# Kernel tuning notes

Measured on AMD Instinct MI355X. Metric: run time of the kernel, lower is better.

Reference implementation:

```python
import jax, jax.numpy as jnp
import numpy as np

N, IN_DIM, ERR_DIM, CAND, NR = 100000, 168, 24, 256, 4

def setup_inputs() -> dict:
    key = jax.random.key(0)
    k1, k2, k3, k4, k5 = jax.random.split(key, 5)
    return {
        "input": jax.random.normal(k1, (N, IN_DIM), dtype=jnp.float32),
        "error": jax.random.normal(k2, (N, ERR_DIM), dtype=jnp.float32),
        "weight_candidates": jax.random.normal(k3, (IN_DIM, CAND), dtype=jnp.float32),
        "bias_candidates": jax.random.normal(k4, (1, CAND), dtype=jnp.float32),
        "r": jax.random.uniform(k5, (NR,), dtype=jnp.float32),
    }

def reference(input, error, weight_candidates, bias_candidates, r):
    # candidates_state: [N, C] = sigmoid(X W + b)
    cand_state = jax.nn.sigmoid(input @ weight_candidates + bias_candidates)
    # E^T C: [D, C]; replaces per-(candidate,dim) tiny mm loop
    ec = jnp.einsum('nd,nc->dc', error, cand_state)
    # c^T c per candidate: [C]
    cc = jnp.sum(cand_state * cand_state, axis=0)
    # left_vector summed over dims: [C]
    left = jnp.sum(ec * ec, axis=0) / cc
    # sum over dims of e_dim^T e_dim: scalar
    ee = jnp.sum(error * error)
    # scores[idx, i] = sum_dim left - (1 - r_i) * right
    scores = left[:, None] - (1.0 - r)[None, :] * ee  # [C, NR]
    return scores
```

## Files before the change

kernel.cpp:

```cpp
#include <hip/hip_runtime.h>


#define N_ROWS 100000
#define IN_DIM 168
#define ERR_DIM 24
#define CAND 256

#define M_TILE 64
#define NT 1563
#define RBLKS 256
#define XT_STRIDE 200
#define ST_STRIDE 72
#define NCOPY 8

typedef __bf16 bf16;
typedef bf16 bf16x4 __attribute__((ext_vector_type(4)));
typedef bf16 bf16x8 __attribute__((ext_vector_type(8)));
typedef float f32x4 __attribute__((ext_vector_type(4)));

#define EC_F 0
#define CC_F 49152
#define EE_F 51200
#define ZERO_N 51456
#define WP_F 51712

__device__ __forceinline__ f32x4 mfma16(bf16x8 a, bf16x8 b, f32x4 c) {
    return __builtin_amdgcn_mfma_f32_16x16x32_bf16(a, b, c, 0, 0, 0);
}

__device__ __forceinline__ float fast_sigmoid(float x) {
    return __builtin_amdgcn_rcpf(1.0f + __expf(-x));
}

__global__ __launch_bounds__(256) void prep_kernel(const float* __restrict__ W,
                                                   bf16* __restrict__ wp,
                                                   float* __restrict__ zero_region) {
    int tid = blockIdx.x * 256 + threadIdx.x;
    for (int i = tid; i < ZERO_N; i += 6144) zero_region[i] = 0.0f;
    int ct  = tid / 384;
    int rem = tid % 384;
    int kt  = rem / 64;
    int l   = rem % 64;
    int c   = ct * 16 + (l & 15);
    int k0  = kt * 32 + (l >> 4) * 8;
    bf16x8 v;
#pragma unroll
    for (int j = 0; j < 8; ++j) {
        int k = k0 + j;
        float f = (k < IN_DIM) ? W[(size_t)k * CAND + c] : 0.0f;
        v[j] = (bf16)f;
    }
    *reinterpret_cast<bf16x8*>(wp + (size_t)tid * 8) = v;
}

__global__ __launch_bounds__(256) void fused_main(const float* __restrict__ X,
                                                  const float* __restrict__ E,
                                                  const float* __restrict__ B,
                                                  const bf16* __restrict__ wp,
                                                  float* __restrict__ ec_ws,
                                                  float* __restrict__ cc_ws,
                                                  float* __restrict__ ee_ws) {
    __shared__ bf16 XT[M_TILE * XT_STRIDE];
    __shared__ bf16 SigT[64 * ST_STRIDE];
    __shared__ bf16 ET[32 * ST_STRIDE];
    __shared__ float red[8];

    const int pid  = blockIdx.x;
    const int cg   = (pid >> 3) >> 5;
    const int rblk = (((pid >> 3) & 31) << 3) | (pid & 7);

    const int tid  = threadIdx.x;
    const int wave = tid >> 6;
    const int lane = tid & 63;
    const int lo   = lane & 15;
    const int hi   = lane >> 4;
    const int ct   = cg * 4 + wave;
    const int cand = ct * 16 + lo;

    bf16x8 wf[6];
#pragma unroll
    for (int kt = 0; kt < 6; ++kt)
        wf[kt] = *reinterpret_cast<const bf16x8*>(wp + (((size_t)(ct * 6 + kt)) * 64 + lane) * 8);
    const float bv = B[cand];

    f32x4 ec_acc[2];
    ec_acc[0] = (f32x4){0.f, 0.f, 0.f, 0.f};
    ec_acc[1] = (f32x4){0.f, 0.f, 0.f, 0.f};
    float cc_acc = 0.f;
    float ee_acc = 0.f;

    for (int i = tid; i < 8 * ST_STRIDE; i += 256)
        ET[(24 + i / ST_STRIDE) * ST_STRIDE + (i % ST_STRIDE)] = (bf16)0.0f;
    {
        bf16x4 z = {(bf16)0.f, (bf16)0.f, (bf16)0.f, (bf16)0.f};
        for (int i = tid; i < 64 * 6; i += 256) {
            int r = i / 6, p = i % 6;
            *reinterpret_cast<bf16x4*>(&XT[r * XT_STRIDE + IN_DIM + p * 4]) = z;
        }
    }

    f32x4 xr[11], er[2];

    auto issue_tile = [&](int tn) {
        const int row0n = tn * M_TILE;
        const bool tval = (tn < NT);
#pragma unroll
        for (int j = 0; j < 11; ++j) {
            int idx = tid + j * 256;
            int r = idx / 42, c4 = idx - r * 42;
            int gr = row0n + r;
            f32x4 v = {0.f, 0.f, 0.f, 0.f};
            if (tval && idx < 2688 && gr < N_ROWS)
                v = *reinterpret_cast<const f32x4*>(X + (size_t)gr * IN_DIM + c4 * 4);
            xr[j] = v;
        }
#pragma unroll
        for (int j = 0; j < 2; ++j) {
            int idx = tid + j * 256;
            int r = idx / 6, p = idx - r * 6;
            int gr = row0n + r;
            f32x4 v = {0.f, 0.f, 0.f, 0.f};
            if (tval && idx < 384 && gr < N_ROWS)
                v = *reinterpret_cast<const f32x4*>(E + (size_t)gr * ERR_DIM + p * 4);
            er[j] = v;
        }
    };

    issue_tile(rblk);

    for (int t = rblk; t < NT; t += RBLKS) {
        const int row0 = t * M_TILE;
        __syncthreads();

#pragma unroll
        for (int j = 0; j < 11; ++j) {
            int idx = tid + j * 256;
            if (idx < 2688) {
                int r = idx / 42, c4 = idx - r * 42;
                f32x4 v = xr[j];
                bf16x4 pk = {(bf16)v.x, (bf16)v.y, (bf16)v.z, (bf16)v.w};
                *reinterpret_cast<bf16x4*>(&XT[r * XT_STRIDE + c4 * 4]) = pk;
            }
        }
#pragma unroll
        for (int j = 0; j < 2; ++j) {
            int idx = tid + j * 256;
            if (idx < 384) {
                int r = idx / 6, p = idx - r * 6;
                f32x4 v = er[j];
                if (cg == 0)
                    ee_acc += v.x * v.x + v.y * v.y + v.z * v.z + v.w * v.w;
                int d0 = p * 4;
                ET[(d0 + 0) * ST_STRIDE + r] = (bf16)v.x;
                ET[(d0 + 1) * ST_STRIDE + r] = (bf16)v.y;
                ET[(d0 + 2) * ST_STRIDE + r] = (bf16)v.z;
                ET[(d0 + 3) * ST_STRIDE + r] = (bf16)v.w;
            }
        }
        __syncthreads();

        issue_tile(t + RBLKS);

        f32x4 acc[4];
#pragma unroll
        for (int mf = 0; mf < 4; ++mf) acc[mf] = (f32x4){0.f, 0.f, 0.f, 0.f};
#pragma unroll
        for (int kt = 0; kt < 6; ++kt) {
            bf16x8 a[4];
#pragma unroll
            for (int mf = 0; mf < 4; ++mf)
                a[mf] = *reinterpret_cast<const bf16x8*>(&XT[(mf * 16 + lo) * XT_STRIDE + kt * 32 + hi * 8]);
#pragma unroll
            for (int mf = 0; mf < 4; ++mf)
                acc[mf] = mfma16(a[mf], wf[kt], acc[mf]);
        }

#pragma unroll
        for (int mf = 0; mf < 4; ++mf) {
            const int rb = row0 + mf * 16 + hi * 4;
            f32x4 v = acc[mf];
            float s0 = fast_sigmoid(v.x + bv);
            float s1 = fast_sigmoid(v.y + bv);
            float s2 = fast_sigmoid(v.z + bv);
            float s3 = fast_sigmoid(v.w + bv);
            if (rb + 0 >= N_ROWS) s0 = 0.0f;
            if (rb + 1 >= N_ROWS) s1 = 0.0f;
            if (rb + 2 >= N_ROWS) s2 = 0.0f;
            if (rb + 3 >= N_ROWS) s3 = 0.0f;
            cc_acc += s0 * s0 + s1 * s1 + s2 * s2 + s3 * s3;
            bf16x4 pk = {(bf16)s0, (bf16)s1, (bf16)s2, (bf16)s3};
            *reinterpret_cast<bf16x4*>(&SigT[(wave * 16 + lo) * ST_STRIDE + mf * 16 + hi * 4]) = pk;
        }

#pragma unroll
        for (int kt2 = 0; kt2 < 2; ++kt2) {
            bf16x8 ea0 = *reinterpret_cast<const bf16x8*>(&ET[(0 * 16 + lo) * ST_STRIDE + kt2 * 32 + hi * 8]);
            bf16x8 ea1 = *reinterpret_cast<const bf16x8*>(&ET[(1 * 16 + lo) * ST_STRIDE + kt2 * 32 + hi * 8]);
            bf16x8 sb  = *reinterpret_cast<const bf16x8*>(&SigT[(wave * 16 + lo) * ST_STRIDE + kt2 * 32 + hi * 8]);
            ec_acc[0] = mfma16(ea0, sb, ec_acc[0]);
            ec_acc[1] = mfma16(ea1, sb, ec_acc[1]);
        }
    }

    const int copy = rblk & (NCOPY - 1);
#pragma unroll
    for (int rf = 0; rf < 2; ++rf)
#pragma unroll
        for (int rr = 0; rr < 4; ++rr) {
            int d = rf * 16 + hi * 4 + rr;
            if (d < ERR_DIM)
                atomicAdd(&ec_ws[copy * (ERR_DIM * CAND) + d * CAND + cand], ec_acc[rf][rr]);
        }
    {
        float v = cc_acc;
        v += __shfl_down(v, 32);
        v += __shfl_down(v, 16);
        if (lane < 16) atomicAdd(&cc_ws[copy * CAND + ct * 16 + lane], v);
    }
    if (cg == 0) {
#pragma unroll
        for (int off = 32; off > 0; off >>= 1) ee_acc += __shfl_down(ee_acc, off);
        if (lane == 0) red[wave] = ee_acc;
    }
    __syncthreads();
    if (cg == 0 && tid == 0) ee_ws[rblk] = red[0] + red[1] + red[2] + red[3];
}

__global__ __launch_bounds__(256) void finalize(const float* __restrict__ ec_ws,
                                                const float* __restrict__ cc_ws,
                                                const float* __restrict__ ee_ws,
                                                const float* __restrict__ r,
                                                float* __restrict__ out) {
    __shared__ float tmp[4];
    __shared__ float s_ee;
    int c = threadIdx.x;
    float p = ee_ws[c];
#pragma unroll
    for (int off = 32; off > 0; off >>= 1) p += __shfl_down(p, off);
    if ((c & 63) == 0) tmp[c >> 6] = p;
    __syncthreads();
    if (c == 0) s_ee = tmp[0] + tmp[1] + tmp[2] + tmp[3];
    __syncthreads();
    float ee = s_ee;
    float ccv = 0.f;
#pragma unroll
    for (int cp = 0; cp < NCOPY; ++cp) ccv += cc_ws[cp * CAND + c];
    float left = 0.f;
#pragma unroll
    for (int d = 0; d < ERR_DIM; ++d) {
        float v = 0.f;
#pragma unroll
        for (int cp = 0; cp < NCOPY; ++cp) v += ec_ws[cp * (ERR_DIM * CAND) + d * CAND + c];
        left += v * v;
    }
    left /= ccv;
#pragma unroll
    for (int i = 0; i < 4; ++i) out[c * 4 + i] = left - (1.0f - r[i]) * ee;
}

extern "C" void kernel_launch(void* const* d_in, const int* in_sizes, int n_in,
                              void* d_out, int out_size, void* d_ws, size_t ws_size,
                              hipStream_t stream) {
    const float* X = (const float*)d_in[0];
    const float* E = (const float*)d_in[1];
    const float* W = (const float*)d_in[2];
    const float* B = (const float*)d_in[3];
    const float* r = (const float*)d_in[4];

    float* wsf   = (float*)d_ws;
    float* ec_ws = wsf + EC_F;
    float* cc_ws = wsf + CC_F;
    float* ee_ws = wsf + EE_F;
    bf16*  wp    = (bf16*)(wsf + WP_F);

    prep_kernel<<<24, 256, 0, stream>>>(W, wp, wsf);
    fused_main<<<4 * RBLKS, 256, 0, stream>>>(X, E, B, wp, ec_ws, cc_ws, ee_ws);
    finalize<<<1, 256, 0, stream>>>(ec_ws, cc_ws, ee_ws, r, (float*)d_out);
}
```

Before: 136.3 us.

## Swap MFMA work split so each wave owns a row block across all candidates

Each wave now computes a 16-row slice for all 64 candidates of its group instead of 64 rows for 16 candidates. It keeps four candidate weight fragment sets in registers and reads one X fragment per k-step, which cuts LDS reads of the X tile by a factor of four. Because the sigmoid tile is now written across waves, a new barrier is added before the E^T·S MFMAs. Register pressure rises (24 bf16x8 weight fragments), which could lower occupancy.

```diff
diff --git a/kernel.cpp b/kernel.cpp
--- a/kernel.cpp
+++ b/kernel.cpp
@@ -74,19 +74,23 @@
     const int lane = tid & 63;
     const int lo   = lane & 15;
     const int hi   = lane >> 4;
-    const int ct   = cg * 4 + wave;
-    const int cand = ct * 16 + lo;
-
-    bf16x8 wf[6];
-#pragma unroll
-    for (int kt = 0; kt < 6; ++kt)
-        wf[kt] = *reinterpret_cast<const bf16x8*>(wp + (((size_t)(ct * 6 + kt)) * 64 + lane) * 8);
-    const float bv = B[cand];
+
+    bf16x8 wf[4][6];
+#pragma unroll
+    for (int cf = 0; cf < 4; ++cf)
+#pragma unroll
+        for (int kt = 0; kt < 6; ++kt)
+            wf[cf][kt] = *reinterpret_cast<const bf16x8*>(
+                wp + (((size_t)((cg * 4 + cf) * 6 + kt)) * 64 + lane) * 8);
+
+    float bv[4];
+#pragma unroll
+    for (int cf = 0; cf < 4; ++cf) bv[cf] = B[cg * 64 + cf * 16 + lo];
 
     f32x4 ec_acc[2];
     ec_acc[0] = (f32x4){0.f, 0.f, 0.f, 0.f};
     ec_acc[1] = (f32x4){0.f, 0.f, 0.f, 0.f};
-    float cc_acc = 0.f;
+    float cc_acc[4] = {0.f, 0.f, 0.f, 0.f};
     float ee_acc = 0.f;
 
     for (int i = tid; i < 8 * ST_STRIDE; i += 256)
@@ -100,7 +104,6 @@
     }
 
     f32x4 xr[11], er[2];
-
     auto issue_tile = [&](int tn) {
         const int row0n = tn * M_TILE;
         const bool tval = (tn < NT);
@@ -163,34 +166,36 @@
 
         f32x4 acc[4];
 #pragma unroll
-        for (int mf = 0; mf < 4; ++mf) acc[mf] = (f32x4){0.f, 0.f, 0.f, 0.f};
+        for (int cf = 0; cf < 4; ++cf) acc[cf] = (f32x4){0.f, 0.f, 0.f, 0.f};
 #pragma unroll
         for (int kt = 0; kt < 6; ++kt) {
-            bf16x8 a[4];
-#pragma unroll
-            for (int mf = 0; mf < 4; ++mf)
-                a[mf] = *reinterpret_cast<const bf16x8*>(&XT[(mf * 16 + lo) * XT_STRIDE + kt * 32 + hi * 8]);
-#pragma unroll
-            for (int mf = 0; mf < 4; ++mf)
-                acc[mf] = mfma16(a[mf], wf[kt], acc[mf]);
-        }
-
-#pragma unroll
-        for (int mf = 0; mf < 4; ++mf) {
-            const int rb = row0 + mf * 16 + hi * 4;
-            f32x4 v = acc[mf];
-            float s0 = fast_sigmoid(v.x + bv);
-            float s1 = fast_sigmoid(v.y + bv);
-            float s2 = fast_sigmoid(v.z + bv);
-            float s3 = fast_sigmoid(v.w + bv);
-            if (rb + 0 >= N_ROWS) s0 = 0.0f;
-            if (rb + 1 >= N_ROWS) s1 = 0.0f;
-            if (rb + 2 >= N_ROWS) s2 = 0.0f;
-            if (rb + 3 >= N_ROWS) s3 = 0.0f;
-            cc_acc += s0 * s0 + s1 * s1 + s2 * s2 + s3 * s3;
-            bf16x4 pk = {(bf16)s0, (bf16)s1, (bf16)s2, (bf16)s3};
-            *reinterpret_cast<bf16x4*>(&SigT[(wave * 16 + lo) * ST_STRIDE + mf * 16 + hi * 4]) = pk;
-        }
+            bf16x8 a = *reinterpret_cast<const bf16x8*>(
+                &XT[(wave * 16 + lo) * XT_STRIDE + kt * 32 + hi * 8]);
+#pragma unroll
+            for (int cf = 0; cf < 4; ++cf)
+                acc[cf] = mfma16(a, wf[cf][kt], acc[cf]);
+        }
+
+        {
+            const int rb = row0 + wave * 16 + hi * 4;
+#pragma unroll
+            for (int cf = 0; cf < 4; ++cf) {
+                f32x4 v = acc[cf];
+                float s0 = fast_sigmoid(v.x + bv[cf]);
+                float s1 = fast_sigmoid(v.y + bv[cf]);
+                float s2 = fast_sigmoid(v.z + bv[cf]);
+                float s3 = fast_sigmoid(v.w + bv[cf]);
+                if (rb + 0 >= N_ROWS) s0 = 0.0f;
+                if (rb + 1 >= N_ROWS) s1 = 0.0f;
+                if (rb + 2 >= N_ROWS) s2 = 0.0f;
+                if (rb + 3 >= N_ROWS) s3 = 0.0f;
+                cc_acc[cf] += s0 * s0 + s1 * s1 + s2 * s2 + s3 * s3;
+                bf16x4 pk = {(bf16)s0, (bf16)s1, (bf16)s2, (bf16)s3};
+                *reinterpret_cast<bf16x4*>(
+                    &SigT[(cf * 16 + lo) * ST_STRIDE + wave * 16 + hi * 4]) = pk;
+            }
+        }
+        __syncthreads();
 
 #pragma unroll
         for (int kt2 = 0; kt2 < 2; ++kt2) {
@@ -209,13 +214,15 @@
         for (int rr = 0; rr < 4; ++rr) {
             int d = rf * 16 + hi * 4 + rr;
             if (d < ERR_DIM)
-                atomicAdd(&ec_ws[copy * (ERR_DIM * CAND) + d * CAND + cand], ec_acc[rf][rr]);
-        }
-    {
-        float v = cc_acc;
+                atomicAdd(&ec_ws[copy * (ERR_DIM * CAND) + d * CAND + cg * 64 + wave * 16 + lo],
+                          ec_acc[rf][rr]);
+        }
+#pragma unroll
+    for (int cf = 0; cf < 4; ++cf) {
+        float v = cc_acc[cf];
         v += __shfl_down(v, 32);
         v += __shfl_down(v, 16);
-        if (lane < 16) atomicAdd(&cc_ws[copy * CAND + ct * 16 + lane], v);
+        if (lane < 16) atomicAdd(&cc_ws[copy * CAND + cg * 64 + cf * 16 + lane], v);
     }
     if (cg == 0) {
 #pragma unroll
```

Measured after the change: 154.5 us. +13.4%, slower.
